# Kernel optimization log

Hardware: AMD Instinct MI355X
Metric: run time of the kernel (lower is better)

Reference implementation:

```python
import jax, jax.numpy as jnp
import numpy as np

TEMPERATURE = 0.1
N, D = 8192, 1024

def setup_inputs() -> dict:
    key = jax.random.key(0)
    k1, k2 = jax.random.split(key)
    im = jax.random.normal(k1, (N, D), dtype=jnp.float32)
    cap = jax.random.normal(k2, (N, D), dtype=jnp.float32)
    return {"im": im, "cap": cap}

def reference(im, cap):
    # InfoNCE (info_nce package) L2-normalizes query, positive and negatives.
    # Per-sample loop: for image i, positive = cap[i], negatives = cap[j != i].
    # Logits set = sim(im_i, cap_j) for all j, positive at j == i, so
    # loss_i = logsumexp_j(S[i, j] / T) - S[i, i] / T  (CLIP-style CE).
    imn = im / jnp.linalg.norm(im, axis=-1, keepdims=True)
    capn = cap / jnp.linalg.norm(cap, axis=-1, keepdims=True)
    S = jnp.einsum('id,jd->ij', imn, capn) / TEMPERATURE  # [N, N]
    diag = jnp.diagonal(S)
    loss_i2c = jax.nn.logsumexp(S, axis=1) - diag  # image -> caption direction
    loss_c2i = jax.nn.logsumexp(S, axis=0) - diag  # caption -> image direction
    # original averages all 2N per-sample losses
    return 0.5 * (jnp.mean(loss_i2c) + jnp.mean(loss_c2i))
```

## Files before the change

### kernel.cpp

```cpp
#include <hip/hip_runtime.h>
#include <stdint.h>

#define N_ 8192
#define D_ 1024
#define EPILOGUE_SCALE (10.0f / 256.0f)
#define ENC_SCALE 16.0f
#define CHUNK 524288

typedef float f32x4 __attribute__((ext_vector_type(4)));
typedef float f32x16 __attribute__((ext_vector_type(16)));
typedef int i32x4 __attribute__((ext_vector_type(4)));
typedef int i32x8 __attribute__((ext_vector_type(8)));

#define GLD16(gsrc, ldst)                                                    \
  __builtin_amdgcn_global_load_lds(                                          \
      (const __attribute__((address_space(1))) unsigned int*)(gsrc),         \
      (__attribute__((address_space(3))) unsigned int*)(ldst), 16, 0, 0)


__global__ __launch_bounds__(256) void normalize_k(
    const float* __restrict__ im, const float* __restrict__ cap,
    unsigned int* __restrict__ imn, unsigned int* __restrict__ capn,
    float* __restrict__ diag, float* __restrict__ sums ) {
  const int b = blockIdx.x;
  const int t = threadIdx.x;
  if (b < 16) ((float4*)sums)[b * 256 + t] = (float4){0.f, 0.f, 0.f, 0.f};

  const int j = t & 63;
  const int row = b * 4 + (t >> 6);
  const float4* __restrict__ aR = (const float4*)(im + (size_t)row * D_);
  const float4* __restrict__ bR = (const float4*)(cap + (size_t)row * D_);

  float4 a0 = aR[j * 4], a1 = aR[j * 4 + 1], a2 = aR[j * 4 + 2], a3 = aR[j * 4 + 3];
  float4 b0 = bR[j * 4], b1 = bR[j * 4 + 1], b2 = bR[j * 4 + 2], b3 = bR[j * 4 + 3];

  float ssa = a0.x * a0.x + a0.y * a0.y + a0.z * a0.z + a0.w * a0.w
            + a1.x * a1.x + a1.y * a1.y + a1.z * a1.z + a1.w * a1.w
            + a2.x * a2.x + a2.y * a2.y + a2.z * a2.z + a2.w * a2.w
            + a3.x * a3.x + a3.y * a3.y + a3.z * a3.z + a3.w * a3.w;
  float ssb = b0.x * b0.x + b0.y * b0.y + b0.z * b0.z + b0.w * b0.w
            + b1.x * b1.x + b1.y * b1.y + b1.z * b1.z + b1.w * b1.w
            + b2.x * b2.x + b2.y * b2.y + b2.z * b2.z + b2.w * b2.w
            + b3.x * b3.x + b3.y * b3.y + b3.z * b3.z + b3.w * b3.w;
  float dt  = a0.x * b0.x + a0.y * b0.y + a0.z * b0.z + a0.w * b0.w
            + a1.x * b1.x + a1.y * b1.y + a1.z * b1.z + a1.w * b1.w
            + a2.x * b2.x + a2.y * b2.y + a2.z * b2.z + a2.w * b2.w
            + a3.x * b3.x + a3.y * b3.y + a3.z * b3.z + a3.w * b3.w;
#pragma unroll
  for (int o = 1; o < 64; o <<= 1) {
    ssa += __shfl_xor(ssa, o, 64);
    ssb += __shfl_xor(ssb, o, 64);
    dt  += __shfl_xor(dt, o, 64);
  }
  const float ra = rsqrtf(ssa), rb = rsqrtf(ssb);
  if (j == 0) diag[row] = dt * ra * rb * 10.0f;
  const float sa = ra * ENC_SCALE, sb = rb * ENC_SCALE;

#define PK(v, s, lo, hi) \
  { lo = __builtin_amdgcn_cvt_pk_fp8_f32(v.x * s, v.y * s, 0, false); \
    lo = __builtin_amdgcn_cvt_pk_fp8_f32(v.z * s, v.w * s, lo, true); (void)hi; }
  int pa0, pa1, pa2, pa3, pb0, pb1, pb2, pb3, dummy;
  PK(a0, sa, pa0, dummy) PK(a1, sa, pa1, dummy)
  PK(a2, sa, pa2, dummy) PK(a3, sa, pa3, dummy)
  PK(b0, sb, pb0, dummy) PK(b1, sb, pb1, dummy)
  PK(b2, sb, pb2, dummy) PK(b3, sb, pb3, dummy)
#undef PK
  uint4 va = {(unsigned)pa0, (unsigned)pa1, (unsigned)pa2, (unsigned)pa3};
  uint4 vb = {(unsigned)pb0, (unsigned)pb1, (unsigned)pb2, (unsigned)pb3};

  {
    const int c = j >> 2, g = (j >> 1) & 1, p = j & 1;
    const size_t d = (size_t)c * CHUNK + (size_t)(row >> 5) * 2048
                   + (size_t)(p << 10) + (size_t)((g << 5) + (row & 31)) * 16;
    *(uint4*)((unsigned char*)imn + d) = va;
    *(uint4*)((unsigned char*)capn + d) = vb;
  }
}

__global__ __launch_bounds__(512, 4) void gemm_lse_k(
    const unsigned char* __restrict__ A,
    const unsigned char* __restrict__ B,
    float* __restrict__ rowsum, float* __restrict__ colsum) {
  __shared__ unsigned char lds[3][24576];
  const int t = threadIdx.x;
  const int w = t >> 6, l = t & 63;
  const int l16 = l * 16;

  const int bid = blockIdx.x + (blockIdx.y << 5);
  const int nid = (bid & 7) * 256 + (bid >> 3);
  const int rowT = ((nid >> 8) << 2) + (nid & 3);
  const int colT = (nid >> 2) & 63;

  const size_t baseA = (size_t)rowT * 16384;
  const size_t baseB = (size_t)colT * 8192;

  const unsigned char* src[3];
  int ldsOff[3];
#pragma unroll
  for (int c = 0; c < 3; ++c) {
    const int o = w * 3072 + c * 1024;
    ldsOff[c] = o;
    src[c] = (o < 16384) ? (A + baseA + o + l16)
                         : (B + baseB + (o - 16384) + l16);
  }

#define STAGE(kc, buf)                                                       \
  {                                                                          \
    const size_t kofs = (size_t)(kc) * CHUNK;                                \
    GLD16(src[0] + kofs, &lds[buf][ldsOff[0]]);                              \
    GLD16(src[1] + kofs, &lds[buf][ldsOff[1]]);                              \
    GLD16(src[2] + kofs, &lds[buf][ldsOff[2]]);                              \
  }

  const int wr = w >> 1, wc = w & 1;

  f32x16 acc[2][2];
#pragma unroll
  for (int m = 0; m < 2; ++m)
#pragma unroll
    for (int n = 0; n < 2; ++n)
#pragma unroll
      for (int r = 0; r < 16; ++r) acc[m][n][r] = 0.f;

#define COMPUTE(buf)                                                         \
  {                                                                          \
    const unsigned char* Lc = &lds[buf][0];                                  \
    i32x8 a_[2], b_[2];                                                      \
    _Pragma("unroll")                                                        \
    for (int m = 0; m < 2; ++m) {                                            \
      i32x4 lo = *(const i32x4*)(Lc + (wr * 2 + m) * 2048 + l16);            \
      i32x4 hi = *(const i32x4*)(Lc + (wr * 2 + m) * 2048 + 1024 + l16);     \
      a_[m] = __builtin_shufflevector(lo, hi, 0, 1, 2, 3, 4, 5, 6, 7);       \
    }                                                                        \
    _Pragma("unroll")                                                        \
    for (int n = 0; n < 2; ++n) {                                            \
      i32x4 lo = *(const i32x4*)(Lc + 16384 + (wc * 2 + n) * 2048 + l16);    \
      i32x4 hi = *(const i32x4*)(Lc + 16384 + (wc * 2 + n) * 2048 + 1024 + l16); \
      b_[n] = __builtin_shufflevector(lo, hi, 0, 1, 2, 3, 4, 5, 6, 7);       \
    }                                                                        \
    __builtin_amdgcn_s_setprio(1);                                           \
    _Pragma("unroll")                                                        \
    for (int m = 0; m < 2; ++m)                                              \
      _Pragma("unroll")                                                      \
      for (int n = 0; n < 2; ++n)                                            \
        acc[m][n] = __builtin_amdgcn_mfma_scale_f32_32x32x64_f8f6f4(         \
            a_[m], b_[n], acc[m][n], 0, 0, 0, 0x7F7F7F7F, 0, 0x7F7F7F7F);    \
    __builtin_amdgcn_s_setprio(0);                                           \
  }

  STAGE(0, 0)
  STAGE(1, 1)

#pragma unroll 1
  for (int kt = 0; kt < 14; ++kt) {
    const int cb = kt % 3, sb = (kt + 2) % 3;
    asm volatile("s_waitcnt vmcnt(3)" ::: "memory");
    __builtin_amdgcn_s_barrier();
    STAGE(kt + 2, sb)
    COMPUTE(cb)
  }
  asm volatile("s_waitcnt vmcnt(3)" ::: "memory");
  __builtin_amdgcn_s_barrier();
  COMPUTE(2)
  asm volatile("s_waitcnt vmcnt(0)" ::: "memory");
  __builtin_amdgcn_s_barrier();
  COMPUTE(0)
#undef COMPUTE
#undef STAGE

#pragma unroll
  for (int m = 0; m < 2; ++m)
#pragma unroll
    for (int n = 0; n < 2; ++n)
#pragma unroll
      for (int r = 0; r < 16; ++r)
        acc[m][n][r] = __expf(acc[m][n][r] * EPILOGUE_SCALE);

  const int rowBase = rowT * 256 + wr * 64;
  const int colBase = colT * 128 + wc * 64;
#pragma unroll
  for (int m = 0; m < 2; ++m) {
    f32x16 s = acc[m][0] + acc[m][1];
#pragma unroll
    for (int r = 0; r < 16; ++r) {
      float v = s[r];
      v += __shfl_xor(v, 1, 64);
      v += __shfl_xor(v, 2, 64);
      v += __shfl_xor(v, 4, 64);
      v += __shfl_xor(v, 8, 64);
      v += __shfl_xor(v, 16, 64);
      if ((l & 31) == 0)
        atomicAdd(&rowsum[rowBase + m * 32 + (r & 3) + 8 * (r >> 2) + 4 * (l >> 5)], v);
    }
  }
#pragma unroll
  for (int n = 0; n < 2; ++n) {
    float v = 0.f;
#pragma unroll
    for (int r = 0; r < 16; ++r) v += acc[0][n][r] + acc[1][n][r];
    v += __shfl_xor(v, 32, 64);
    if (l < 32)
      atomicAdd(&colsum[colBase + n * 32 + l], v);
  }
}

__global__ __launch_bounds__(256) void finalize_k(
    const float* __restrict__ rowsum, const float* __restrict__ colsum,
    const float* __restrict__ diag, float* __restrict__ out) {
  const int t = threadIdx.x;
  float lse = 0.f, dg = 0.f;
  for (int i = t; i < N_; i += 256) {
    lse += __logf(rowsum[i]) + __logf(colsum[i]);
    dg += diag[i];
  }
#pragma unroll
  for (int o = 32; o > 0; o >>= 1) {
    lse += __shfl_down(lse, o, 64);
    dg  += __shfl_down(dg, o, 64);
  }
  __shared__ float red[2][4];
  const int w = t >> 6, l = t & 63;
  if (l == 0) { red[0][w] = lse; red[1][w] = dg; }
  __syncthreads();
  if (t == 0) {
    lse = red[0][0] + red[0][1] + red[0][2] + red[0][3];
    dg  = red[1][0] + red[1][1] + red[1][2] + red[1][3];
    out[0] = 0.5f * lse / (float)N_ - dg / (float)N_;
  }
}

extern "C" void kernel_launch(void* const* d_in, const int* in_sizes, int n_in,
                              void* d_out, int out_size, void* d_ws, size_t ws_size,
                              hipStream_t stream) {
  const float* im = (const float*)d_in[0];
  const float* cap = (const float*)d_in[1];
  float* out = (float*)d_out;
  char* ws = (char*)d_ws;
  unsigned char* imn = (unsigned char*)ws;
  unsigned char* capn = imn + (size_t)N_ * D_;
  float* rowsum = (float*)(ws + 2 * (size_t)N_ * D_);
  float* colsum = rowsum + N_;
  float* diag = colsum + N_;

  normalize_k<<<2048, 256, 0, stream>>>(im, cap, (unsigned int*)imn,
                                        (unsigned int*)capn, diag, rowsum);
  gemm_lse_k<<<dim3(32, 64), 512, 0, stream>>>(imn, capn, rowsum, colsum);
  finalize_k<<<1, 256, 0, stream>>>(rowsum, colsum, diag, out);
}
```

Baseline: 198.3 us.

## Make GEMM blocks persistent over four column tiles and fuse finalize via last-block counter

The GEMM grid drops from 2048 blocks to 512. Each block now loops over four consecutive 128-column tiles, running the epilogue (exp, row/col reductions, atomics) after every 16 K-chunks and keeping the load pipeline streaming across tile boundaries. The separate finalize kernel is removed: a global counter, zeroed in normalize_k, lets the last block to finish compute the final loss. This saves one launch and avoids per-block prologue and pipeline-drain costs. In exchange, only 512 blocks run, which can mean fewer waves to balance across CUs, and the epilogues inside the loop stall the pipeline.

```diff
diff --git a/kernel.cpp b/kernel.cpp
--- a/kernel.cpp
+++ b/kernel.cpp
@@ -21,10 +21,12 @@
 __global__ __launch_bounds__(256) void normalize_k(
     const float* __restrict__ im, const float* __restrict__ cap,
     unsigned int* __restrict__ imn, unsigned int* __restrict__ capn,
-    float* __restrict__ diag, float* __restrict__ sums ) {
+    float* __restrict__ diag, float* __restrict__ sums ,
+    unsigned int* __restrict__ cnt) {
   const int b = blockIdx.x;
   const int t = threadIdx.x;
   if (b < 16) ((float4*)sums)[b * 256 + t] = (float4){0.f, 0.f, 0.f, 0.f};
+  if (b == 0 && t == 0) *cnt = 0u;
 
   const int j = t & 63;
   const int row = b * 4 + (t >> 6);
@@ -56,14 +58,12 @@
   if (j == 0) diag[row] = dt * ra * rb * 10.0f;
   const float sa = ra * ENC_SCALE, sb = rb * ENC_SCALE;
 
-#define PK(v, s, lo, hi) \
+#define PK(v, s, lo) \
   { lo = __builtin_amdgcn_cvt_pk_fp8_f32(v.x * s, v.y * s, 0, false); \
-    lo = __builtin_amdgcn_cvt_pk_fp8_f32(v.z * s, v.w * s, lo, true); (void)hi; }
-  int pa0, pa1, pa2, pa3, pb0, pb1, pb2, pb3, dummy;
-  PK(a0, sa, pa0, dummy) PK(a1, sa, pa1, dummy)
-  PK(a2, sa, pa2, dummy) PK(a3, sa, pa3, dummy)
-  PK(b0, sb, pb0, dummy) PK(b1, sb, pb1, dummy)
-  PK(b2, sb, pb2, dummy) PK(b3, sb, pb3, dummy)
+    lo = __builtin_amdgcn_cvt_pk_fp8_f32(v.z * s, v.w * s, lo, true); }
+  int pa0, pa1, pa2, pa3, pb0, pb1, pb2, pb3;
+  PK(a0, sa, pa0) PK(a1, sa, pa1) PK(a2, sa, pa2) PK(a3, sa, pa3)
+  PK(b0, sb, pb0) PK(b1, sb, pb1) PK(b2, sb, pb2) PK(b3, sb, pb3)
 #undef PK
   uint4 va = {(unsigned)pa0, (unsigned)pa1, (unsigned)pa2, (unsigned)pa3};
   uint4 vb = {(unsigned)pb0, (unsigned)pb1, (unsigned)pb2, (unsigned)pb3};
@@ -80,36 +80,41 @@
 __global__ __launch_bounds__(512, 4) void gemm_lse_k(
     const unsigned char* __restrict__ A,
     const unsigned char* __restrict__ B,
-    float* __restrict__ rowsum, float* __restrict__ colsum) {
+    float* __restrict__ rowsum, float* __restrict__ colsum,
+    const float* __restrict__ diag, float* __restrict__ out,
+    unsigned int* __restrict__ cnt) {
   __shared__ unsigned char lds[3][24576];
+  __shared__ unsigned int lastFlag;
+  __shared__ float red[2][8];
   const int t = threadIdx.x;
   const int w = t >> 6, l = t & 63;
   const int l16 = l * 16;
 
-  const int bid = blockIdx.x + (blockIdx.y << 5);
-  const int nid = (bid & 7) * 256 + (bid >> 3);
-  const int rowT = ((nid >> 8) << 2) + (nid & 3);
-  const int colT = (nid >> 2) & 63;
+  const int bid = blockIdx.x;
+  const int nid = (bid & 7) * 64 + (bid >> 3);
+  const int rowT = ((nid >> 6) << 2) + (nid & 3);
+  const int colG = (nid >> 2) & 15;
 
   const size_t baseA = (size_t)rowT * 16384;
-  const size_t baseB = (size_t)colT * 8192;
-
-  const unsigned char* src[3];
-  int ldsOff[3];
+  const size_t baseB = (size_t)colG * 32768;
+
+  const unsigned char* srcc[3];
+  int bstr[3], ldsOff[3];
 #pragma unroll
   for (int c = 0; c < 3; ++c) {
     const int o = w * 3072 + c * 1024;
     ldsOff[c] = o;
-    src[c] = (o < 16384) ? (A + baseA + o + l16)
-                         : (B + baseB + (o - 16384) + l16);
-  }
-
-#define STAGE(kc, buf)                                                       \
+    if (o < 16384) { srcc[c] = A + baseA + o + l16;           bstr[c] = 0; }
+    else           { srcc[c] = B + baseB + (o - 16384) + l16; bstr[c] = 8192; }
+  }
+
+#define STAGE(kk, buf)                                                       \
   {                                                                          \
-    const size_t kofs = (size_t)(kc) * CHUNK;                                \
-    GLD16(src[0] + kofs, &lds[buf][ldsOff[0]]);                              \
-    GLD16(src[1] + kofs, &lds[buf][ldsOff[1]]);                              \
-    GLD16(src[2] + kofs, &lds[buf][ldsOff[2]]);                              \
+    const int kc_ = (kk) & 15, tt_ = (kk) >> 4;                              \
+    const size_t kofs = (size_t)kc_ * CHUNK;                                 \
+    GLD16(srcc[0] + kofs + (size_t)tt_ * bstr[0], &lds[buf][ldsOff[0]]);     \
+    GLD16(srcc[1] + kofs + (size_t)tt_ * bstr[1], &lds[buf][ldsOff[1]]);     \
+    GLD16(srcc[2] + kofs + (size_t)tt_ * bstr[2], &lds[buf][ldsOff[2]]);     \
   }
 
   const int wr = w >> 1, wc = w & 1;
@@ -148,16 +153,60 @@
     __builtin_amdgcn_s_setprio(0);                                           \
   }
 
+#define EPILOGUE(tt_)                                                        \
+  {                                                                          \
+    _Pragma("unroll")                                                        \
+    for (int m = 0; m < 2; ++m)                                              \
+      _Pragma("unroll")                                                      \
+      for (int n = 0; n < 2; ++n)                                            \
+        _Pragma("unroll")                                                    \
+        for (int r = 0; r < 16; ++r)                                         \
+          acc[m][n][r] = __expf(acc[m][n][r] * EPILOGUE_SCALE);              \
+    const int rowBase = rowT * 256 + wr * 64;                                \
+    const int colBase = (colG * 4 + (tt_)) * 128 + wc * 64;                  \
+    _Pragma("unroll")                                                        \
+    for (int m = 0; m < 2; ++m) {                                            \
+      f32x16 s = acc[m][0] + acc[m][1];                                      \
+      _Pragma("unroll")                                                      \
+      for (int r = 0; r < 16; ++r) {                                         \
+        float v = s[r];                                                      \
+        v += __shfl_xor(v, 1, 64);                                           \
+        v += __shfl_xor(v, 2, 64);                                           \
+        v += __shfl_xor(v, 4, 64);                                           \
+        v += __shfl_xor(v, 8, 64);                                           \
+        v += __shfl_xor(v, 16, 64);                                          \
+        if ((l & 31) == 0)                                                   \
+          atomicAdd(&rowsum[rowBase + m * 32 + (r & 3) + 8 * (r >> 2)        \
+                            + 4 * (l >> 5)], v);                             \
+      }                                                                      \
+    }                                                                        \
+    _Pragma("unroll")                                                        \
+    for (int n = 0; n < 2; ++n) {                                            \
+      float v = 0.f;                                                         \
+      _Pragma("unroll")                                                      \
+      for (int r = 0; r < 16; ++r) v += acc[0][n][r] + acc[1][n][r];         \
+      v += __shfl_xor(v, 32, 64);                                            \
+      if (l < 32) atomicAdd(&colsum[colBase + n * 32 + l], v);               \
+    }                                                                        \
+    _Pragma("unroll")                                                        \
+    for (int m = 0; m < 2; ++m)                                              \
+      _Pragma("unroll")                                                      \
+      for (int n = 0; n < 2; ++n)                                            \
+        _Pragma("unroll")                                                    \
+        for (int r = 0; r < 16; ++r) acc[m][n][r] = 0.f;                     \
+  }
+
   STAGE(0, 0)
   STAGE(1, 1)
 
+  int tt = 0;
 #pragma unroll 1
-  for (int kt = 0; kt < 14; ++kt) {
-    const int cb = kt % 3, sb = (kt + 2) % 3;
+  for (int kk = 0; kk < 62; ++kk) {
     asm volatile("s_waitcnt vmcnt(3)" ::: "memory");
     __builtin_amdgcn_s_barrier();
-    STAGE(kt + 2, sb)
-    COMPUTE(cb)
+    STAGE(kk + 2, (kk + 2) % 3)
+    COMPUTE(kk % 3)
+    if ((kk & 15) == 15) { EPILOGUE(tt) ++tt; }
   }
   asm volatile("s_waitcnt vmcnt(3)" ::: "memory");
   __builtin_amdgcn_s_barrier();
@@ -165,67 +214,41 @@
   asm volatile("s_waitcnt vmcnt(0)" ::: "memory");
   __builtin_amdgcn_s_barrier();
   COMPUTE(0)
+  EPILOGUE(3)
+#undef EPILOGUE
 #undef COMPUTE
 #undef STAGE
 
-#pragma unroll
-  for (int m = 0; m < 2; ++m)
-#pragma unroll
-    for (int n = 0; n < 2; ++n)
-#pragma unroll
-      for (int r = 0; r < 16; ++r)
-        acc[m][n][r] = __expf(acc[m][n][r] * EPILOGUE_SCALE);
-
-  const int rowBase = rowT * 256 + wr * 64;
-  const int colBase = colT * 128 + wc * 64;
-#pragma unroll
-  for (int m = 0; m < 2; ++m) {
-    f32x16 s = acc[m][0] + acc[m][1];
-#pragma unroll
-    for (int r = 0; r < 16; ++r) {
-      float v = s[r];
-      v += __shfl_xor(v, 1, 64);
-      v += __shfl_xor(v, 2, 64);
-      v += __shfl_xor(v, 4, 64);
-      v += __shfl_xor(v, 8, 64);
-      v += __shfl_xor(v, 16, 64);
-      if ((l & 31) == 0)
-        atomicAdd(&rowsum[rowBase + m * 32 + (r & 3) + 8 * (r >> 2) + 4 * (l >> 5)], v);
+  __threadfence();
+  if (t == 0) lastFlag = (atomicAdd(cnt, 1u) == 511u) ? 1u : 0u;
+  __syncthreads();
+  if (lastFlag) {
+    __threadfence();
+    float lse = 0.f, dg = 0.f;
+    for (int i = t; i < N_; i += 512) {
+      const float rs = __hip_atomic_load(&rowsum[i], __ATOMIC_RELAXED,
+                                         __HIP_MEMORY_SCOPE_AGENT);
+      const float cs = __hip_atomic_load(&colsum[i], __ATOMIC_RELAXED,
+                                         __HIP_MEMORY_SCOPE_AGENT);
+      const float dd = __hip_atomic_load(&diag[i], __ATOMIC_RELAXED,
+                                         __HIP_MEMORY_SCOPE_AGENT);
+      lse += __logf(rs) + __logf(cs);
+      dg += dd;
     }
-  }
-#pragma unroll
-  for (int n = 0; n < 2; ++n) {
-    float v = 0.f;
-#pragma unroll
-    for (int r = 0; r < 16; ++r) v += acc[0][n][r] + acc[1][n][r];
-    v += __shfl_xor(v, 32, 64);
-    if (l < 32)
-      atomicAdd(&colsum[colBase + n * 32 + l], v);
-  }
-}
-
-__global__ __launch_bounds__(256) void finalize_k(
-    const float* __restrict__ rowsum, const float* __restrict__ colsum,
-    const float* __restrict__ diag, float* __restrict__ out) {
-  const int t = threadIdx.x;
-  float lse = 0.f, dg = 0.f;
-  for (int i = t; i < N_; i += 256) {
-    lse += __logf(rowsum[i]) + __logf(colsum[i]);
-    dg += diag[i];
-  }
-#pragma unroll
-  for (int o = 32; o > 0; o >>= 1) {
-    lse += __shfl_down(lse, o, 64);
-    dg  += __shfl_down(dg, o, 64);
-  }
-  __shared__ float red[2][4];
-  const int w = t >> 6, l = t & 63;
-  if (l == 0) { red[0][w] = lse; red[1][w] = dg; }
-  __syncthreads();
-  if (t == 0) {
-    lse = red[0][0] + red[0][1] + red[0][2] + red[0][3];
-    dg  = red[1][0] + red[1][1] + red[1][2] + red[1][3];
-    out[0] = 0.5f * lse / (float)N_ - dg / (float)N_;
+#pragma unroll
+    for (int o = 32; o > 0; o >>= 1) {
+      lse += __shfl_down(lse, o, 64);
+      dg  += __shfl_down(dg, o, 64);
+    }
+    if (l == 0) { red[0][w] = lse; red[1][w] = dg; }
+    __syncthreads();
+    if (t == 0) {
+      lse = red[0][0] + red[0][1] + red[0][2] + red[0][3]
+          + red[0][4] + red[0][5] + red[0][6] + red[0][7];
+      dg  = red[1][0] + red[1][1] + red[1][2] + red[1][3]
+          + red[1][4] + red[1][5] + red[1][6] + red[1][7];
+      out[0] = 0.5f * lse / (float)N_ - dg / (float)N_;
+    }
   }
 }
 
@@ -241,9 +264,9 @@
   float* rowsum = (float*)(ws + 2 * (size_t)N_ * D_);
   float* colsum = rowsum + N_;
   float* diag = colsum + N_;
+  unsigned int* cnt = (unsigned int*)(diag + N_);
 
   normalize_k<<<2048, 256, 0, stream>>>(im, cap, (unsigned int*)imn,
-                                        (unsigned int*)capn, diag, rowsum);
-  gemm_lse_k<<<dim3(32, 64), 512, 0, stream>>>(imn, capn, rowsum, colsum);
-  finalize_k<<<1, 256, 0, stream>>>(rowsum, colsum, diag, out);
+                                        (unsigned int*)capn, diag, rowsum, cnt);
+  gemm_lse_k<<<512, 512, 0, stream>>>(imn, capn, rowsum, colsum, diag, out, cnt);
 }
```

After: 254.5 us. +28.3%, slower.
